# Performance work log

Measured on AMD Instinct MI355X. Metric: run time of the kernel, lower is better.

The kernel has to match this reference:

```python
import jax, jax.numpy as jnp
import numpy as np

N = 20000          # nodes
E = 200000         # edges
IN = 256           # in_channels
OUT = 256          # out_channels (heads * per-head)
H = 2              # heads
C = OUT // 2       # per-head channels (out_channels // 2)
TDIM = 100         # time_enc.out_channels
MSG = 156          # msg_dim
EDGE_DIM = TDIM + MSG  # 256
P = 0.1            # dropout prob


def setup_inputs() -> dict:
    key = jax.random.key(0)
    ks = jax.random.split(key, 20)
    s = 1.0 / np.sqrt(IN)
    se = 1.0 / np.sqrt(EDGE_DIM)
    return {
        "x": jax.random.normal(ks[0], (N, IN), jnp.float32),
        "last_update": jax.random.uniform(ks[1], (N,), jnp.float32) * 100.0,
        "edge_index": jax.random.randint(ks[2], (2, E), 0, N, jnp.int64),
        "t": jax.random.uniform(ks[3], (E,), jnp.float32) * 100.0,
        "msg": jax.random.normal(ks[4], (E, MSG), jnp.float32),
        "u_edge": jax.random.uniform(ks[5], (E,), jnp.float32),
        "u_attn": jax.random.uniform(ks[6], (E, H), jnp.float32),
        # TimeEncoder: cos(Linear(1, TDIM))
        "time_w": jax.random.normal(ks[7], (TDIM,), jnp.float32),
        "time_b": jax.random.normal(ks[8], (TDIM,), jnp.float32) * 0.1,
        # TransformerConv params ([in, out] layout)
        "Wq": jax.random.normal(ks[9], (IN, H * C), jnp.float32) * s,
        "bq": jnp.zeros((H * C,), jnp.float32),
        "Wk": jax.random.normal(ks[10], (IN, H * C), jnp.float32) * s,
        "bk": jnp.zeros((H * C,), jnp.float32),
        "Wv": jax.random.normal(ks[11], (IN, H * C), jnp.float32) * s,
        "bv": jnp.zeros((H * C,), jnp.float32),
        "We": jax.random.normal(ks[12], (EDGE_DIM, H * C), jnp.float32) * se,
        "be": jnp.zeros((H * C,), jnp.float32),
        "Ws": jax.random.normal(ks[13], (IN, H * C), jnp.float32) * s,
        "bs": jnp.zeros((H * C,), jnp.float32),
    }


def reference(x, last_update, edge_index, t, msg, u_edge, u_attn,
              time_w, time_b, Wq, bq, Wk, bk, Wv, bv, We, be, Ws, bs):
    src, dst = edge_index[0], edge_index[1]
    # time encoding of relative time (TGN TimeEncoder: cos(Linear(1, TDIM)))
    rel_t = last_update[src] - t                              # [E]
    rel_enc = jnp.cos(rel_t[:, None] * time_w[None, :] + time_b)  # [E, TDIM]
    edge_attr = jnp.concatenate([rel_enc, msg], axis=-1)      # [E, EDGE_DIM]
    # dropout_adj: drop edges with prob P (no rescale)
    keep = u_edge > P                                         # [E] bool

    q = (x @ Wq + bq).reshape(N, H, C)
    k = (x @ Wk + bk).reshape(N, H, C)
    v = (x @ Wv + bv).reshape(N, H, C)
    e = (edge_attr @ We + be).reshape(E, H, C)

    kj = k[src] + e                                           # [E, H, C]
    alpha = jnp.einsum('ehc,ehc->eh', q[dst], kj) / jnp.sqrt(jnp.float32(C))
    alpha = jnp.where(keep[:, None], alpha, -jnp.inf)
    # segment softmax over incoming edges of each dst node
    m = jax.ops.segment_max(alpha, dst, num_segments=N)       # [N, H]
    m = jnp.where(jnp.isfinite(m), m, 0.0)
    ex = jnp.where(keep[:, None], jnp.exp(alpha - m[dst]), 0.0)
    denom = jax.ops.segment_sum(ex, dst, num_segments=N)      # [N, H]
    attn = ex / (denom[dst] + 1e-16)                          # [E, H]
    # attention dropout (post-softmax, inverted scaling)
    attn = attn * (u_attn > P).astype(attn.dtype) / (1.0 - P)

    msg_out = (v[src] + e) * attn[:, :, None]                 # [E, H, C]
    out = jax.ops.segment_sum(msg_out, dst, num_segments=N).reshape(N, H * C)
    # root/skip connection
    return out + (x @ Ws + bs)
```

## Files before the change

### kernel.cpp

```cpp
#include <hip/hip_runtime.h>

#define NND 20000
#define NE 200000
#define PDROP 0.1f

typedef unsigned short u16;
typedef __bf16 bf16x8 __attribute__((ext_vector_type(8)));
typedef float f32x4 __attribute__((ext_vector_type(4)));

__device__ __forceinline__ float b2f(u16 u) {
  unsigned v = ((unsigned)u) << 16;
  float f;
  __builtin_memcpy(&f, &v, 4);
  return f;
}
__device__ __forceinline__ u16 f2b(float f) {
  unsigned x;
  __builtin_memcpy(&x, &f, 4);
  unsigned r = x + 0x7fffu + ((x >> 16) & 1u);
  return (u16)(r >> 16);
}

struct WTArgs {
  const float* W[5];
  u16* WT[5];
};

__global__ __launch_bounds__(256) void prep(const float* __restrict__ x,
                                            u16* __restrict__ xb, WTArgs a,
                                            const float* __restrict__ msg,
                                            u16* __restrict__ msgb,
                                            int* __restrict__ cnt,
                                            int* __restrict__ cur) {
  const int b = blockIdx.x, tid = threadIdx.x;
  if (b < 30469) {
    int i = b * 256 + tid;
    if (i < 7800000) {
      float4 v = ((const float4*)msg)[i];
      ushort4 o;
      o.x = f2b(v.x); o.y = f2b(v.y); o.z = f2b(v.z); o.w = f2b(v.w);
      ((ushort4*)msgb)[i] = o;
    }
  } else if (b < 35469) {
    int i = (b - 30469) * 256 + tid;
    float4 v = ((const float4*)x)[i];
    ushort4 o;
    o.x = f2b(v.x); o.y = f2b(v.y); o.z = f2b(v.z); o.w = f2b(v.w);
    ((ushort4*)xb)[i] = o;
  } else if (b < 36749) {
    int gid = (b - 35469) * 256 + tid;
    int w = gid >> 16, r = gid & 65535;
    int n = r >> 8, k = r & 255;
    a.WT[w][n * 256 + k] = f2b(a.W[w][k * 256 + n]);
  } else {
    int i = (b - 36749) * 256 + tid;
    if (i < NND) { cnt[i] = 0; cur[i] = 0; }
  }
}

__global__ void wprep(const float* __restrict__ Wq, const float* __restrict__ We,
                      const float* __restrict__ bq, u16* __restrict__ WcT,
                      float* __restrict__ qwe_bias) {
  int gid = blockIdx.x * blockDim.x + threadIdx.x;
  if (gid < 131072) {
    int i = gid & 255, j = gid >> 8;
    int h = j >> 8, jj = j & 255;
    float acc = 0.f;
#pragma unroll 4
    for (int c = 0; c < 128; c++)
      acc += Wq[i * 256 + h * 128 + c] * We[jj * 256 + h * 128 + c];
    WcT[j * 256 + i] = f2b(acc);
  } else if (gid < 131584) {
    int j = gid - 131072;
    int h = j >> 8, jj = j & 255;
    float acc = 0.f;
#pragma unroll 4
    for (int c = 0; c < 128; c++)
      acc += bq[h * 128 + c] * We[jj * 256 + h * 128 + c];
    qwe_bias[j] = acc;
  }
}

__global__ void csr_count(const int* __restrict__ ei, int* __restrict__ cnt) {
  int e = blockIdx.x * blockDim.x + threadIdx.x;
  if (e < NE) atomicAdd(&cnt[ei[NE + e]], 1);
}
__global__ __launch_bounds__(1024) void scan_rowptr(const int* __restrict__ cnt,
                                                    int* __restrict__ rowptr) {
  __shared__ int sums[1024];
  const int tid = threadIdx.x;
  const int base = tid * 20;
  int local[20];
  int run = 0;
#pragma unroll
  for (int i = 0; i < 20; i++) {
    int idx = base + i;
    local[i] = run;
    run += (idx < NND) ? cnt[idx] : 0;
  }
  sums[tid] = run;
  __syncthreads();
  for (int off = 1; off < 1024; off <<= 1) {
    int v = (tid >= off) ? sums[tid - off] : 0;
    __syncthreads();
    sums[tid] += v;
    __syncthreads();
  }
  int prev = (tid > 0) ? sums[tid - 1] : 0;
#pragma unroll
  for (int i = 0; i < 20; i++) {
    int idx = base + i;
    if (idx < NND) rowptr[idx] = prev + local[i];
  }
  if (tid == 1023) rowptr[NND] = sums[1023];
}

__global__ void csr_fill(const int* __restrict__ ei,
                         const float* __restrict__ last_update,
                         const float* __restrict__ t,
                         const float* __restrict__ u_edge,
                         const float* __restrict__ u_attn,
                         const int* __restrict__ rowptr, int* __restrict__ cur,
                         uint4* __restrict__ recs) {
  int e = blockIdx.x * blockDim.x + threadIdx.x;
  if (e < NE) {
    int s = ei[e];
    int d = ei[NE + e];
    int p = rowptr[d] + atomicAdd(&cur[d], 1);
    bool keep = u_edge[e] > PDROP;
    float rt = last_update[s] - t[e];
    float2 ua = *(const float2*)&u_attn[(size_t)e * 2];
    uint4 r;
    r.x = (unsigned)s | (keep ? 0u : 0x80000000u);
    r.y = __float_as_uint(rt);
    r.z = (unsigned)e | ((ua.x > PDROP) ? 0x40000000u : 0u) |
          ((ua.y > PDROP) ? 0x80000000u : 0u);
    r.w = 0u;
    recs[p] = r;
  }
}

__device__ __forceinline__ void mfma_tile(const u16 (*As)[72], const u16 (*Bs)[72],
                                          f32x4 acc[4][4], int wm, int wn,
                                          int fr, int fg) {
#pragma unroll
  for (int ks = 0; ks < 2; ks++) {
    bf16x8 a[4], b[4];
#pragma unroll
    for (int i = 0; i < 4; i++)
      a[i] = *(const bf16x8*)&As[wm * 64 + i * 16 + fr][ks * 32 + fg * 8];
#pragma unroll
    for (int j = 0; j < 4; j++)
      b[j] = *(const bf16x8*)&Bs[wn * 64 + j * 16 + fr][ks * 32 + fg * 8];
#pragma unroll
    for (int i = 0; i < 4; i++)
#pragma unroll
      for (int j = 0; j < 4; j++)
        acc[i][j] = __builtin_amdgcn_mfma_f32_16x16x32_bf16(a[i], b[j], acc[i][j], 0, 0, 0);
  }
}

struct NodeArgs {
  const u16* BT[6];
  const float* bias[6];
  u16* outb[3];
  float* outf;
  u16* qWeb;
};
__global__ __launch_bounds__(256) void gemm_node(const u16* __restrict__ xb,
                                                 NodeArgs args) {
  __shared__ __attribute__((aligned(16))) u16 As[128][72];
  __shared__ __attribute__((aligned(16))) u16 Bs[128][72];
  const int tid = threadIdx.x;
  const int w = blockIdx.y >> 1;
  const int col0 = (blockIdx.y & 1) * 128;
  const int row0 = blockIdx.x * 128;
  const u16* BT = args.BT[w];
  const float* bias = args.bias[w];
  const int wid = tid >> 6, lane = tid & 63;
  const int wm = wid >> 1, wn = wid & 1;
  const int fr = lane & 15, fg = lane >> 4;
  f32x4 acc[4][4] = {};
  for (int k0 = 0; k0 < 256; k0 += 64) {
#pragma unroll
    for (int i = 0; i < 4; i++) {
      int idx = tid + i * 256;
      int row = idx >> 3, vc = idx & 7;
      int g = row0 + row;
      uint4 v = make_uint4(0, 0, 0, 0);
      if (g < NND) v = *(const uint4*)&xb[(size_t)g * 256 + k0 + vc * 8];
      *(uint4*)&As[row][vc * 8] = v;
      *(uint4*)&Bs[row][vc * 8] = *(const uint4*)&BT[(size_t)(col0 + row) * 256 + k0 + vc * 8];
    }
    __syncthreads();
    mfma_tile(As, Bs, acc, wm, wn, fr, fg);
    __syncthreads();
  }
#pragma unroll
  for (int mi = 0; mi < 4; mi++) {
#pragma unroll
    for (int rr = 0; rr < 4; rr++) {
      int grow = row0 + wm * 64 + mi * 16 + fg * 4 + rr;
      if (grow >= NND) continue;
#pragma unroll
      for (int ni = 0; ni < 4; ni++) {
        int gcol = col0 + wn * 64 + ni * 16 + fr;
        float val = acc[mi][ni][rr] + bias[gcol];
        if (w < 3)
          args.outb[w][(size_t)grow * 256 + gcol] = f2b(val);
        else if (w == 3)
          args.outf[(size_t)grow * 256 + gcol] = val;
        else
          args.qWeb[(size_t)grow * 512 + (w - 4) * 256 + gcol] = f2b(val);
      }
    }
  }
}

__global__ __launch_bounds__(256) void node_fused(
    const u16* __restrict__ qb, const u16* __restrict__ kb,
    const u16* __restrict__ vb, const u16* __restrict__ qWeb,
    const u16* __restrict__ msgb, const float* __restrict__ tw,
    const float* __restrict__ tb_, const float* __restrict__ be,
    const int* __restrict__ rowptr, const uint4* __restrict__ recs,
    u16* __restrict__ aggb, float* __restrict__ out) {
  const int node = (blockIdx.x * blockDim.x + threadIdx.x) >> 6;
  const int lane = threadIdx.x & 63;
  if (node >= NND) return;
  const int beg = rowptr[node], end = rowptr[node + 1];
  const int c0 = lane * 4, hl = lane >> 5;

  ushort4 q4 = *(const ushort4*)&qb[(size_t)node * 256 + c0];
  float qf0 = b2f(q4.x), qf1 = b2f(q4.y), qf2 = b2f(q4.z), qf3 = b2f(q4.w);
  ushort4 w0v = *(const ushort4*)&qWeb[(size_t)node * 512 + c0];
  ushort4 w1v = *(const ushort4*)&qWeb[(size_t)node * 512 + 256 + c0];
  float qw00 = b2f(w0v.x), qw01 = b2f(w0v.y), qw02 = b2f(w0v.z), qw03 = b2f(w0v.w);
  float qw10 = b2f(w1v.x), qw11 = b2f(w1v.y), qw12 = b2f(w1v.z), qw13 = b2f(w1v.w);
  float4 bev = *(const float4*)&be[c0];
  float pb = qf0 * bev.x + qf1 * bev.y + qf2 * bev.z + qf3 * bev.w;
#pragma unroll
  for (int off = 16; off; off >>= 1) pb += __shfl_xor(pb, off);
  float tw0 = 0, tw1 = 0, tw2 = 0, tw3 = 0, tb0 = 0, tb1 = 0, tb2 = 0, tb3 = 0;
  if (c0 < 100) {
    float4 a = *(const float4*)&tw[c0];
    float4 b = *(const float4*)&tb_[c0];
    tw0 = a.x; tw1 = a.y; tw2 = a.z; tw3 = a.w;
    tb0 = b.x; tb1 = b.y; tb2 = b.z; tb3 = b.w;
  }
  const float inv = 0.08838834764831845f;

  float m0 = -INFINITY, m1 = -INFINITY;
  float den0 = 0.f, den1 = 0.f, sw0 = 0.f, sw1 = 0.f;
  float vc0 = 0, vc1 = 0, vc2 = 0, vc3 = 0;
  float g00 = 0, g01 = 0, g02 = 0, g03 = 0;
  float g10 = 0, g11 = 0, g12 = 0, g13 = 0;

  for (int j0 = beg; j0 < end; j0 += 4) {
    float ea[4][4];
    unsigned se[4];
    float rt[4], wk0[4], wk1[4];
    ushort4 k4[4], v4[4], mm4[4];
#pragma unroll
    for (int e = 0; e < 4; ++e) {
      int j = j0 + e;
      int jc = (j < end) ? j : (end - 1);
      uint4 rr = recs[jc];
      bool valid = (j < end);
      se[e] = valid ? rr.x : 0xFFFFFFFFu;
      rt[e] = __uint_as_float(rr.y);
      unsigned rz = rr.z;
      wk0[e] = (valid && (rz & 0x40000000u)) ? (1.f / 0.9f) : 0.f;
      wk1[e] = (valid && (rz & 0x80000000u)) ? (1.f / 0.9f) : 0.f;
      int s_ = (int)(rr.x & 0x7fffffffu);
      k4[e] = *(const ushort4*)&kb[(size_t)s_ * 256 + c0];
      v4[e] = *(const ushort4*)&vb[(size_t)s_ * 256 + c0];
      if (c0 >= 100) {
        int eid = (int)(rz & 0x3FFFFFFFu);
        mm4[e] = *(const ushort4*)&msgb[(size_t)eid * 156 + (c0 - 100)];
      }
    }
    if (c0 < 100) {
#pragma unroll
      for (int e = 0; e < 4; ++e) {
        ea[e][0] = __cosf(rt[e] * tw0 + tb0);
        ea[e][1] = __cosf(rt[e] * tw1 + tb1);
        ea[e][2] = __cosf(rt[e] * tw2 + tb2);
        ea[e][3] = __cosf(rt[e] * tw3 + tb3);
      }
    } else {
#pragma unroll
      for (int e = 0; e < 4; ++e) {
        ea[e][0] = b2f(mm4[e].x); ea[e][1] = b2f(mm4[e].y);
        ea[e][2] = b2f(mm4[e].z); ea[e][3] = b2f(mm4[e].w);
      }
    }
    float zq[4];
#pragma unroll
    for (int e = 0; e < 4; ++e) {
      float pq = qf0 * b2f(k4[e].x) + qf1 * b2f(k4[e].y) +
                 qf2 * b2f(k4[e].z) + qf3 * b2f(k4[e].w);
      float pe0 = qw00 * ea[e][0] + qw01 * ea[e][1] + qw02 * ea[e][2] + qw03 * ea[e][3];
      float pe1 = qw10 * ea[e][0] + qw11 * ea[e][1] + qw12 * ea[e][2] + qw13 * ea[e][3];
      float y0 = pe0 + __shfl_xor(pe0, 32);
      float y1 = pe1 + __shfl_xor(pe1, 32);
      zq[e] = ((lane < 32) ? y0 : y1) + pq;
    }
#pragma unroll
    for (int off = 16; off; off >>= 1) {
#pragma unroll
      for (int e = 0; e < 4; ++e) zq[e] += __shfl_xor(zq[e], off);
    }
    float a0[4], a1[4];
#pragma unroll
    for (int e = 0; e < 4; ++e) {
      float a = (se[e] < 0x80000000u) ? (zq[e] + pb) * inv : -INFINITY;
      float aoth = __shfl_xor(a, 32);
      a0[e] = (lane < 32) ? a : aoth;
      a1[e] = (lane < 32) ? aoth : a;
    }
    float cm0 = fmaxf(fmaxf(a0[0], a0[1]), fmaxf(a0[2], a0[3]));
    float cm1 = fmaxf(fmaxf(a1[0], a1[1]), fmaxf(a1[2], a1[3]));
    if (cm0 > m0) {
      float sc = (m0 > -1e30f) ? __expf(m0 - cm0) : 0.f;
      den0 *= sc; sw0 *= sc;
      g00 *= sc; g01 *= sc; g02 *= sc; g03 *= sc;
      float scv = hl ? 1.f : sc;
      vc0 *= scv; vc1 *= scv; vc2 *= scv; vc3 *= scv;
      m0 = cm0;
    }
    if (cm1 > m1) {
      float sc = (m1 > -1e30f) ? __expf(m1 - cm1) : 0.f;
      den1 *= sc; sw1 *= sc;
      g10 *= sc; g11 *= sc; g12 *= sc; g13 *= sc;
      float scv = hl ? sc : 1.f;
      vc0 *= scv; vc1 *= scv; vc2 *= scv; vc3 *= scv;
      m1 = cm1;
    }
#pragma unroll
    for (int e = 0; e < 4; ++e) {
      float ex0 = (a0[e] > -1e30f) ? __expf(a0[e] - m0) : 0.f;
      float ex1 = (a1[e] > -1e30f) ? __expf(a1[e] - m1) : 0.f;
      den0 += ex0; den1 += ex1;
      float w0 = ex0 * wk0[e], w1 = ex1 * wk1[e];
      float wv = hl ? w1 : w0;
      vc0 += wv * b2f(v4[e].x); vc1 += wv * b2f(v4[e].y);
      vc2 += wv * b2f(v4[e].z); vc3 += wv * b2f(v4[e].w);
      g00 += w0 * ea[e][0]; g01 += w0 * ea[e][1];
      g02 += w0 * ea[e][2]; g03 += w0 * ea[e][3];
      g10 += w1 * ea[e][0]; g11 += w1 * ea[e][1];
      g12 += w1 * ea[e][2]; g13 += w1 * ea[e][3];
      sw0 += w0; sw1 += w1;
    }
  }

  float rden0 = 1.f / (den0 + 1e-16f), rden1 = 1.f / (den1 + 1e-16f);
  float rv = hl ? rden1 : rden0;
  float swv = hl ? sw1 : sw0;
  float4 o = *(float4*)&out[(size_t)node * 256 + c0];
  o.x += (vc0 + swv * bev.x) * rv;
  o.y += (vc1 + swv * bev.y) * rv;
  o.z += (vc2 + swv * bev.z) * rv;
  o.w += (vc3 + swv * bev.w) * rv;
  *(float4*)&out[(size_t)node * 256 + c0] = o;
  ushort4 a0v, a1v;
  a0v.x = f2b(g00 * rden0); a0v.y = f2b(g01 * rden0);
  a0v.z = f2b(g02 * rden0); a0v.w = f2b(g03 * rden0);
  a1v.x = f2b(g10 * rden1); a1v.y = f2b(g11 * rden1);
  a1v.z = f2b(g12 * rden1); a1v.w = f2b(g13 * rden1);
  *(ushort4*)&aggb[(size_t)node * 256 + c0] = a0v;
  *(ushort4*)&aggb[(size_t)(NND + node) * 256 + c0] = a1v;
}

__global__ __launch_bounds__(256) void gemm_final(const u16* __restrict__ aggb,
                                                  const u16* __restrict__ WeT,
                                                  float* __restrict__ out) {
  __shared__ __attribute__((aligned(16))) u16 As[128][72];
  __shared__ __attribute__((aligned(16))) u16 Bs[128][72];
  const int tid = threadIdx.x;
  const int h = blockIdx.y;
  const int row0 = blockIdx.x * 128;
  const u16* A = aggb + (size_t)h * NND * 256;
  const int wid = tid >> 6, lane = tid & 63;
  const int wm = wid >> 1, wn = wid & 1;
  const int fr = lane & 15, fg = lane >> 4;
  f32x4 acc[4][4] = {};
  for (int k0 = 0; k0 < 256; k0 += 64) {
#pragma unroll
    for (int i = 0; i < 4; i++) {
      int idx = tid + i * 256;
      int row = idx >> 3, vc = idx & 7;
      int g = row0 + row;
      uint4 v = make_uint4(0, 0, 0, 0);
      if (g < NND) v = *(const uint4*)&A[(size_t)g * 256 + k0 + vc * 8];
      *(uint4*)&As[row][vc * 8] = v;
      *(uint4*)&Bs[row][vc * 8] =
          *(const uint4*)&WeT[(size_t)(h * 128 + row) * 256 + k0 + vc * 8];
    }
    __syncthreads();
    mfma_tile(As, Bs, acc, wm, wn, fr, fg);
    __syncthreads();
  }
#pragma unroll
  for (int mi = 0; mi < 4; mi++) {
#pragma unroll
    for (int rr = 0; rr < 4; rr++) {
      int grow = row0 + wm * 64 + mi * 16 + fg * 4 + rr;
      if (grow >= NND) continue;
#pragma unroll
      for (int ni = 0; ni < 4; ni++) {
        int gcol = wn * 64 + ni * 16 + fr;
        out[(size_t)grow * 256 + h * 128 + gcol] += acc[mi][ni][rr];
      }
    }
  }
}

extern "C" void kernel_launch(void* const* d_in, const int* in_sizes, int n_in,
                              void* d_out, int out_size, void* d_ws, size_t ws_size,
                              hipStream_t stream) {
  const float* x = (const float*)d_in[0];
  const float* last_update = (const float*)d_in[1];
  const int* ei = (const int*)d_in[2];
  const float* t = (const float*)d_in[3];
  const float* msg = (const float*)d_in[4];
  const float* u_edge = (const float*)d_in[5];
  const float* u_attn = (const float*)d_in[6];
  const float* time_w = (const float*)d_in[7];
  const float* time_b = (const float*)d_in[8];
  const float* Wq = (const float*)d_in[9];
  const float* bq = (const float*)d_in[10];
  const float* Wk = (const float*)d_in[11];
  const float* bk = (const float*)d_in[12];
  const float* Wv = (const float*)d_in[13];
  const float* bv = (const float*)d_in[14];
  const float* We = (const float*)d_in[15];
  const float* be = (const float*)d_in[16];
  const float* Ws = (const float*)d_in[17];
  const float* bs = (const float*)d_in[18];
  float* out = (float*)d_out;

  char* ws = (char*)d_ws;
  u16* xb = (u16*)(ws + 0);
  u16* WT0 = (u16*)(ws + 10240000);
  u16* WcT = (u16*)(ws + 10895360);
  float* qwe_bias = (float*)(ws + 11157504);
  u16* qb = (u16*)(ws + 11159552);
  u16* kb = (u16*)(ws + 21399552);
  u16* vb = (u16*)(ws + 31639552);
  u16* qWeb = (u16*)(ws + 41879552);
  u16* aggb = (u16*)(ws + 62359552);
  uint4* recs = (uint4*)(ws + 82839552);
  u16* msgb = (u16*)(ws + 86039552);
  int* cnt = (int*)(ws + 148439552);
  int* cur = (int*)(ws + 148519552);
  int* rowptr = (int*)(ws + 148599552);

  WTArgs wa;
  wa.W[0] = Wq; wa.W[1] = Wk; wa.W[2] = Wv; wa.W[3] = Ws; wa.W[4] = We;
  for (int i = 0; i < 5; i++) wa.WT[i] = WT0 + (size_t)i * 65536;
  prep<<<36828, 256, 0, stream>>>(x, xb, wa, msg, msgb, cnt, cur);

  wprep<<<514, 256, 0, stream>>>(Wq, We, bq, WcT, qwe_bias);

  csr_count<<<(NE + 255) / 256, 256, 0, stream>>>(ei, cnt);
  scan_rowptr<<<1, 1024, 0, stream>>>(cnt, rowptr);
  csr_fill<<<(NE + 255) / 256, 256, 0, stream>>>(ei, last_update, t, u_edge,
                                                 u_attn, rowptr, cur, recs);

  NodeArgs na;
  na.BT[0] = wa.WT[0]; na.BT[1] = wa.WT[1]; na.BT[2] = wa.WT[2]; na.BT[3] = wa.WT[3];
  na.BT[4] = WcT; na.BT[5] = WcT + 256 * 256;
  na.bias[0] = bq; na.bias[1] = bk; na.bias[2] = bv; na.bias[3] = bs;
  na.bias[4] = qwe_bias; na.bias[5] = qwe_bias + 256;
  na.outb[0] = qb; na.outb[1] = kb; na.outb[2] = vb;
  na.outf = out;
  na.qWeb = qWeb;
  dim3 gn((NND + 127) / 128, 12);
  gemm_node<<<gn, 256, 0, stream>>>(xb, na);

  node_fused<<<(NND + 3) / 4, 256, 0, stream>>>(
      qb, kb, vb, qWeb, msgb, time_w, time_b, be, rowptr, recs, aggb, out);

  dim3 gf((NND + 127) / 128, 2);
  gemm_final<<<gf, 256, 0, stream>>>(aggb, wa.WT[4], out);
}
```

Baseline: 265.8 us.

## Fold skip GEMM into final GEMM and merge prep, wprep and count kernels

Merges the weight-combine (wprep) and edge-count (csr_count) kernels into the prep launch, and replaces the in-kernel zeroing of cnt and cur with one hipMemsetAsync. The skip-connection GEMM (x @ Ws) moves from gemm_node into the final GEMM, which now writes the output once. node_fused writes its value-aggregation result as a bf16 buffer instead of doing a read-modify-write on the fp32 output, and gets an occupancy launch bound. This removes two launches and the fp32 output round-trips. In exchange, the msg conversion now runs one wavefront per edge with only 39 of 64 lanes active, and the value-aggregate term is rounded to bf16 before being added.

```diff
diff --git a/kernel.cpp b/kernel.cpp
--- a/kernel.cpp
+++ b/kernel.cpp
@@ -26,65 +26,60 @@
   u16* WT[5];
 };
 
-__global__ __launch_bounds__(256) void prep(const float* __restrict__ x,
-                                            u16* __restrict__ xb, WTArgs a,
-                                            const float* __restrict__ msg,
-                                            u16* __restrict__ msgb,
-                                            int* __restrict__ cnt,
-                                            int* __restrict__ cur) {
+__global__ __launch_bounds__(256) void prep(
+    const float* __restrict__ msg, u16* __restrict__ msgb,
+    const float* __restrict__ x, u16* __restrict__ xb, WTArgs a,
+    const int* __restrict__ ei, int* __restrict__ cnt,
+    const float* __restrict__ Wq, const float* __restrict__ We,
+    const float* __restrict__ bq, u16* __restrict__ WcT,
+    float* __restrict__ qwe_bias) {
   const int b = blockIdx.x, tid = threadIdx.x;
-  if (b < 30469) {
-    int i = b * 256 + tid;
-    if (i < 7800000) {
-      float4 v = ((const float4*)msg)[i];
+  if (b < 50000) {
+    int e = b * 4 + (tid >> 6);
+    int lane = tid & 63;
+    int c = lane * 4;
+    if (c < 156) {
+      float4 v = *(const float4*)&msg[(size_t)e * 156 + c];
       ushort4 o;
       o.x = f2b(v.x); o.y = f2b(v.y); o.z = f2b(v.z); o.w = f2b(v.w);
-      ((ushort4*)msgb)[i] = o;
-    }
-  } else if (b < 35469) {
-    int i = (b - 30469) * 256 + tid;
+      *(ushort4*)&msgb[(size_t)e * 156 + c] = o;
+    }
+  } else if (b < 55000) {
+    int i = (b - 50000) * 256 + tid;
     float4 v = ((const float4*)x)[i];
     ushort4 o;
     o.x = f2b(v.x); o.y = f2b(v.y); o.z = f2b(v.z); o.w = f2b(v.w);
     ((ushort4*)xb)[i] = o;
-  } else if (b < 36749) {
-    int gid = (b - 35469) * 256 + tid;
+  } else if (b < 56280) {
+    int gid = (b - 55000) * 256 + tid;
     int w = gid >> 16, r = gid & 65535;
     int n = r >> 8, k = r & 255;
     a.WT[w][n * 256 + k] = f2b(a.W[w][k * 256 + n]);
+  } else if (b < 57062) {
+    int e = (b - 56280) * 256 + tid;
+    if (e < NE) atomicAdd(&cnt[ei[NE + e]], 1);
   } else {
-    int i = (b - 36749) * 256 + tid;
-    if (i < NND) { cnt[i] = 0; cur[i] = 0; }
-  }
-}
-
-__global__ void wprep(const float* __restrict__ Wq, const float* __restrict__ We,
-                      const float* __restrict__ bq, u16* __restrict__ WcT,
-                      float* __restrict__ qwe_bias) {
-  int gid = blockIdx.x * blockDim.x + threadIdx.x;
-  if (gid < 131072) {
-    int i = gid & 255, j = gid >> 8;
-    int h = j >> 8, jj = j & 255;
-    float acc = 0.f;
+    int gid = (b - 57062) * 256 + tid;
+    if (gid < 131072) {
+      int i = gid & 255, j = gid >> 8;
+      int h = j >> 8, jj = j & 255;
+      float acc = 0.f;
 #pragma unroll 4
-    for (int c = 0; c < 128; c++)
-      acc += Wq[i * 256 + h * 128 + c] * We[jj * 256 + h * 128 + c];
-    WcT[j * 256 + i] = f2b(acc);
-  } else if (gid < 131584) {
-    int j = gid - 131072;
-    int h = j >> 8, jj = j & 255;
-    float acc = 0.f;
+      for (int c = 0; c < 128; c++)
+        acc += Wq[i * 256 + h * 128 + c] * We[jj * 256 + h * 128 + c];
+      WcT[j * 256 + i] = f2b(acc);
+    } else {
+      int j = gid - 131072;
+      int h = j >> 8, jj = j & 255;
+      float acc = 0.f;
 #pragma unroll 4
-    for (int c = 0; c < 128; c++)
-      acc += bq[h * 128 + c] * We[jj * 256 + h * 128 + c];
-    qwe_bias[j] = acc;
-  }
-}
-
-__global__ void csr_count(const int* __restrict__ ei, int* __restrict__ cnt) {
-  int e = blockIdx.x * blockDim.x + threadIdx.x;
-  if (e < NE) atomicAdd(&cnt[ei[NE + e]], 1);
-}
+      for (int c = 0; c < 128; c++)
+        acc += bq[h * 128 + c] * We[jj * 256 + h * 128 + c];
+      qwe_bias[j] = acc;
+    }
+  }
+}
+
 __global__ __launch_bounds__(1024) void scan_rowptr(const int* __restrict__ cnt,
                                                     int* __restrict__ rowptr) {
   __shared__ int sums[1024];
@@ -161,10 +156,9 @@
 }
 
 struct NodeArgs {
-  const u16* BT[6];
-  const float* bias[6];
+  const u16* BT[5];
+  const float* bias[5];
   u16* outb[3];
-  float* outf;
   u16* qWeb;
 };
 __global__ __launch_bounds__(256) void gemm_node(const u16* __restrict__ xb,
@@ -208,22 +202,20 @@
         float val = acc[mi][ni][rr] + bias[gcol];
         if (w < 3)
           args.outb[w][(size_t)grow * 256 + gcol] = f2b(val);
-        else if (w == 3)
-          args.outf[(size_t)grow * 256 + gcol] = val;
         else
-          args.qWeb[(size_t)grow * 512 + (w - 4) * 256 + gcol] = f2b(val);
+          args.qWeb[(size_t)grow * 512 + (w - 3) * 256 + gcol] = f2b(val);
       }
     }
   }
 }
 
-__global__ __launch_bounds__(256) void node_fused(
+__global__ __launch_bounds__(256, 8) void node_fused(
     const u16* __restrict__ qb, const u16* __restrict__ kb,
     const u16* __restrict__ vb, const u16* __restrict__ qWeb,
     const u16* __restrict__ msgb, const float* __restrict__ tw,
     const float* __restrict__ tb_, const float* __restrict__ be,
     const int* __restrict__ rowptr, const uint4* __restrict__ recs,
-    u16* __restrict__ aggb, float* __restrict__ out) {
+    u16* __restrict__ aggb, u16* __restrict__ vaggb) {
   const int node = (blockIdx.x * blockDim.x + threadIdx.x) >> 6;
   const int lane = threadIdx.x & 63;
   if (node >= NND) return;
@@ -259,7 +251,7 @@
     float ea[4][4];
     unsigned se[4];
     float rt[4], wk0[4], wk1[4];
-    ushort4 k4[4], v4[4], mm4[4];
+    ushort4 k4[4], v4[4];
 #pragma unroll
     for (int e = 0; e < 4; ++e) {
       int j = j0 + e;
@@ -276,7 +268,9 @@
       v4[e] = *(const ushort4*)&vb[(size_t)s_ * 256 + c0];
       if (c0 >= 100) {
         int eid = (int)(rz & 0x3FFFFFFFu);
-        mm4[e] = *(const ushort4*)&msgb[(size_t)eid * 156 + (c0 - 100)];
+        ushort4 mm = *(const ushort4*)&msgb[(size_t)eid * 156 + (c0 - 100)];
+        ea[e][0] = b2f(mm.x); ea[e][1] = b2f(mm.y);
+        ea[e][2] = b2f(mm.z); ea[e][3] = b2f(mm.w);
       }
     }
     if (c0 < 100) {
@@ -286,12 +280,6 @@
         ea[e][1] = __cosf(rt[e] * tw1 + tb1);
         ea[e][2] = __cosf(rt[e] * tw2 + tb2);
         ea[e][3] = __cosf(rt[e] * tw3 + tb3);
-      }
-    } else {
-#pragma unroll
-      for (int e = 0; e < 4; ++e) {
-        ea[e][0] = b2f(mm4[e].x); ea[e][1] = b2f(mm4[e].y);
-        ea[e][2] = b2f(mm4[e].z); ea[e][3] = b2f(mm4[e].w);
       }
     }
     float zq[4];
@@ -356,12 +344,12 @@
   float rden0 = 1.f / (den0 + 1e-16f), rden1 = 1.f / (den1 + 1e-16f);
   float rv = hl ? rden1 : rden0;
   float swv = hl ? sw1 : sw0;
-  float4 o = *(float4*)&out[(size_t)node * 256 + c0];
-  o.x += (vc0 + swv * bev.x) * rv;
-  o.y += (vc1 + swv * bev.y) * rv;
-  o.z += (vc2 + swv * bev.z) * rv;
-  o.w += (vc3 + swv * bev.w) * rv;
-  *(float4*)&out[(size_t)node * 256 + c0] = o;
+  ushort4 vg;
+  vg.x = f2b((vc0 + swv * bev.x) * rv);
+  vg.y = f2b((vc1 + swv * bev.y) * rv);
+  vg.z = f2b((vc2 + swv * bev.z) * rv);
+  vg.w = f2b((vc3 + swv * bev.w) * rv);
+  *(ushort4*)&vaggb[(size_t)node * 256 + c0] = vg;
   ushort4 a0v, a1v;
   a0v.x = f2b(g00 * rden0); a0v.y = f2b(g01 * rden0);
   a0v.z = f2b(g02 * rden0); a0v.w = f2b(g03 * rden0);
@@ -371,15 +359,16 @@
   *(ushort4*)&aggb[(size_t)(NND + node) * 256 + c0] = a1v;
 }
 
-__global__ __launch_bounds__(256) void gemm_final(const u16* __restrict__ aggb,
-                                                  const u16* __restrict__ WeT,
-                                                  float* __restrict__ out) {
+__global__ __launch_bounds__(256) void gemm_final2(
+    const u16* __restrict__ xb, const u16* __restrict__ aggb,
+    const u16* __restrict__ WsT, const u16* __restrict__ WeT,
+    const float* __restrict__ bs, const u16* __restrict__ vaggb,
+    float* __restrict__ out) {
   __shared__ __attribute__((aligned(16))) u16 As[128][72];
   __shared__ __attribute__((aligned(16))) u16 Bs[128][72];
   const int tid = threadIdx.x;
   const int h = blockIdx.y;
   const int row0 = blockIdx.x * 128;
-  const u16* A = aggb + (size_t)h * NND * 256;
   const int wid = tid >> 6, lane = tid & 63;
   const int wm = wid >> 1, wn = wid & 1;
   const int fr = lane & 15, fg = lane >> 4;
@@ -391,7 +380,24 @@
       int row = idx >> 3, vc = idx & 7;
       int g = row0 + row;
       uint4 v = make_uint4(0, 0, 0, 0);
-      if (g < NND) v = *(const uint4*)&A[(size_t)g * 256 + k0 + vc * 8];
+      if (g < NND) v = *(const uint4*)&xb[(size_t)g * 256 + k0 + vc * 8];
+      *(uint4*)&As[row][vc * 8] = v;
+      *(uint4*)&Bs[row][vc * 8] =
+          *(const uint4*)&WsT[(size_t)(h * 128 + row) * 256 + k0 + vc * 8];
+    }
+    __syncthreads();
+    mfma_tile(As, Bs, acc, wm, wn, fr, fg);
+    __syncthreads();
+  }
+  const u16* A2 = aggb + (size_t)h * NND * 256;
+  for (int k0 = 0; k0 < 256; k0 += 64) {
+#pragma unroll
+    for (int i = 0; i < 4; i++) {
+      int idx = tid + i * 256;
+      int row = idx >> 3, vc = idx & 7;
+      int g = row0 + row;
+      uint4 v = make_uint4(0, 0, 0, 0);
+      if (g < NND) v = *(const uint4*)&A2[(size_t)g * 256 + k0 + vc * 8];
       *(uint4*)&As[row][vc * 8] = v;
       *(uint4*)&Bs[row][vc * 8] =
           *(const uint4*)&WeT[(size_t)(h * 128 + row) * 256 + k0 + vc * 8];
@@ -409,7 +415,9 @@
 #pragma unroll
       for (int ni = 0; ni < 4; ni++) {
         int gcol = wn * 64 + ni * 16 + fr;
-        out[(size_t)grow * 256 + h * 128 + gcol] += acc[mi][ni][rr];
+        int oc = h * 128 + gcol;
+        out[(size_t)grow * 256 + oc] =
+            acc[mi][ni][rr] + bs[oc] + b2f(vaggb[(size_t)grow * 256 + oc]);
       }
     }
   }
@@ -449,38 +457,39 @@
   u16* vb = (u16*)(ws + 31639552);
   u16* qWeb = (u16*)(ws + 41879552);
   u16* aggb = (u16*)(ws + 62359552);
-  uint4* recs = (uint4*)(ws + 82839552);
-  u16* msgb = (u16*)(ws + 86039552);
-  int* cnt = (int*)(ws + 148439552);
-  int* cur = (int*)(ws + 148519552);
-  int* rowptr = (int*)(ws + 148599552);
+  u16* vaggb = (u16*)(ws + 82839552);
+  uint4* recs = (uint4*)(ws + 93079552);
+  u16* msgb = (u16*)(ws + 96279552);
+  int* cnt = (int*)(ws + 158679552);
+  int* cur = (int*)(ws + 158759552);
+  int* rowptr = (int*)(ws + 158839552);
 
   WTArgs wa;
   wa.W[0] = Wq; wa.W[1] = Wk; wa.W[2] = Wv; wa.W[3] = Ws; wa.W[4] = We;
   for (int i = 0; i < 5; i++) wa.WT[i] = WT0 + (size_t)i * 65536;
-  prep<<<36828, 256, 0, stream>>>(x, xb, wa, msg, msgb, cnt, cur);
-
-  wprep<<<514, 256, 0, stream>>>(Wq, We, bq, WcT, qwe_bias);
-
-  csr_count<<<(NE + 255) / 256, 256, 0, stream>>>(ei, cnt);
+
+  hipMemsetAsync(cnt, 0, 160000, stream);
+  prep<<<57576, 256, 0, stream>>>(msg, msgb, x, xb, wa, ei, cnt, Wq, We, bq,
+                                  WcT, qwe_bias);
+
   scan_rowptr<<<1, 1024, 0, stream>>>(cnt, rowptr);
   csr_fill<<<(NE + 255) / 256, 256, 0, stream>>>(ei, last_update, t, u_edge,
                                                  u_attn, rowptr, cur, recs);
 
   NodeArgs na;
-  na.BT[0] = wa.WT[0]; na.BT[1] = wa.WT[1]; na.BT[2] = wa.WT[2]; na.BT[3] = wa.WT[3];
-  na.BT[4] = WcT; na.BT[5] = WcT + 256 * 256;
-  na.bias[0] = bq; na.bias[1] = bk; na.bias[2] = bv; na.bias[3] = bs;
-  na.bias[4] = qwe_bias; na.bias[5] = qwe_bias + 256;
+  na.BT[0] = wa.WT[0]; na.BT[1] = wa.WT[1]; na.BT[2] = wa.WT[2];
+  na.BT[3] = WcT; na.BT[4] = WcT + 256 * 256;
+  na.bias[0] = bq; na.bias[1] = bk; na.bias[2] = bv;
+  na.bias[3] = qwe_bias; na.bias[4] = qwe_bias + 256;
   na.outb[0] = qb; na.outb[1] = kb; na.outb[2] = vb;
-  na.outf = out;
   na.qWeb = qWeb;
-  dim3 gn((NND + 127) / 128, 12);
+  dim3 gn((NND + 127) / 128, 10);
   gemm_node<<<gn, 256, 0, stream>>>(xb, na);
 
   node_fused<<<(NND + 3) / 4, 256, 0, stream>>>(
-      qb, kb, vb, qWeb, msgb, time_w, time_b, be, rowptr, recs, aggb, out);
+      qb, kb, vb, qWeb, msgb, time_w, time_b, be, rowptr, recs, aggb, vaggb);
 
   dim3 gf((NND + 127) / 128, 2);
-  gemm_final<<<gf, 256, 0, stream>>>(aggb, wa.WT[4], out);
-}
+  gemm_final2<<<gf, 256, 0, stream>>>(xb, aggb, wa.WT[3], wa.WT[4], bs, vaggb,
+                                      out);
+}
```

Measured after the change: 524.9 us. +97.5%, slower.
